# Kernel tuning notes

Measured on AMD Instinct MI355X. Metric: run time of the kernel, lower is better.

Reference implementation:

```python
import jax, jax.numpy as jnp
import numpy as np

NUM_HEADS = 16
HEAD_DIM = 64


def setup_inputs() -> dict:
    key = jax.random.key(0)
    ks = jax.random.split(key, 6)
    B, S, E = 4, 1024, 1024
    return {
        "x": jax.random.normal(ks[0], (B, S, E), dtype=jnp.float32),
        "W_qkv": jax.random.normal(ks[1], (E, 3 * E), dtype=jnp.float32) * 0.02,
        "b_qkv": jax.random.normal(ks[2], (3 * E,), dtype=jnp.float32) * 0.02,
        "pe": jax.random.normal(ks[3], (S, S, HEAD_DIM), dtype=jnp.float32) * 0.02,
        "W_out": jax.random.normal(ks[4], (E, E), dtype=jnp.float32) * 0.02,
        "b_out": jax.random.normal(ks[5], (E,), dtype=jnp.float32) * 0.02,
    }


def reference(x, W_qkv, b_qkv, pe, W_out, b_out):
    B, S, E = x.shape
    H, D = NUM_HEADS, HEAD_DIM
    scale = D ** -0.5
    # qkv projection: (B,S,3E) -> (3,B,H,S,D)
    qkv = (x @ W_qkv + b_qkv).reshape(B, S, 3, H, D).transpose(2, 0, 3, 1, 4)
    q, k, v = qkv[0], qkv[1], qkv[2]
    # raw scaled scores (NO softmax in original module)
    scores = jnp.einsum('bhxd,bhyd->bhxy', q, k) * scale
    # relative position bias: pe is (S,S,D) == (x,y,c); original permutes to (c,x,y)
    # then einsum('cxy,bnxc->bnxy', pe, q) -> equivalent to 'xyc,bhxc->bhxy'
    pe_q = jnp.einsum('xyc,bhxc->bhxy', pe, q) * scale
    attn = (scores + pe_q) @ v                      # (B,H,S,D)
    out = attn.transpose(0, 2, 1, 3).reshape(B, S, E)
    return out @ W_out + b_out
```

## Files before the change

### kernel.cpp

```cpp
#include <hip/hip_runtime.h>
#include <cstdint>
#include <cstddef>


typedef unsigned short u16;
typedef __bf16 bf16x8 __attribute__((ext_vector_type(8)));
typedef float  f32x4  __attribute__((ext_vector_type(4)));
typedef unsigned short u16x8 __attribute__((ext_vector_type(8)));

#define MFMA16(a, b, c) __builtin_amdgcn_mfma_f32_16x16x32_bf16((a), (b), (c), 0, 0, 0)

__device__ __forceinline__ u16 f2bf(float f) {
    __bf16 h = (__bf16)f;
    return __builtin_bit_cast(u16, h);
}
__device__ __forceinline__ float bf2f(u16 u) {
    unsigned int x = ((unsigned int)u) << 16;
    return __builtin_bit_cast(float, x);
}
__device__ __forceinline__ u16x8 pack8(float4 a, float4 b) {
    u16x8 v;
    v[0] = f2bf(a.x); v[1] = f2bf(a.y); v[2] = f2bf(a.z); v[3] = f2bf(a.w);
    v[4] = f2bf(b.x); v[5] = f2bf(b.y); v[6] = f2bf(b.z); v[7] = f2bf(b.w);
    return v;
}

__global__ __launch_bounds__(256) void kconv_T(const float* __restrict__ in,
                                               u16* __restrict__ out, int R, int C) {
    __shared__ float tile[64][68];
    const int t  = threadIdx.x;
    const int r0 = blockIdx.y * 64, c0 = blockIdx.x * 64;
    const int rr = t >> 4, c4 = t & 15;
    for (int p = 0; p < 4; ++p) {
        int r = rr + p * 16;
        float4 v = *(const float4*)&in[(size_t)(r0 + r) * C + c0 + c4 * 4];
        *(float4*)&tile[r][c4 * 4] = v;
    }
    __syncthreads();
    for (int p = 0; p < 4; ++p) {
        int n = rr + p * 16;
        ushort4 o;
        o.x = f2bf(tile[c4 * 4 + 0][n]);
        o.y = f2bf(tile[c4 * 4 + 1][n]);
        o.z = f2bf(tile[c4 * 4 + 2][n]);
        o.w = f2bf(tile[c4 * 4 + 3][n]);
        *(ushort4*)&out[(size_t)(c0 + n) * R + r0 + c4 * 4] = o;
    }
}

__global__ __launch_bounds__(256, 3) void kgemm_qkv(const float* __restrict__ X,
                                                    const u16* __restrict__ WT,
                                                    const float* __restrict__ bias,
                                                    u16* __restrict__ qb,
                                                    u16* __restrict__ kb,
                                                    u16* __restrict__ vb) {
    __shared__ u16 a_s[128 * 72];
    __shared__ u16 b_s[128 * 72];
    const int t = threadIdx.x;
    const int m0 = blockIdx.y * 128, n0 = blockIdx.x * 128;
    const int lane = t & 63, w = t >> 6, lm = lane & 15, lq = lane >> 4;
    const int mb = (w >> 1) * 64, nb = (w & 1) * 64;
    const int srow = t >> 3, scc = t & 7;

    f32x4 acc[4][4] = {};
    for (int k0 = 0; k0 < 1024; k0 += 64) {
        __syncthreads();
        for (int p = 0; p < 4; ++p) {
            int r = srow + p * 32;
            const float* src = &X[(size_t)(m0 + r) * 1024 + k0 + scc * 8];
            float4 f0 = *(const float4*)&src[0];
            float4 f1 = *(const float4*)&src[4];
            *(u16x8*)&a_s[r * 72 + scc * 8] = pack8(f0, f1);
        }
        for (int p = 0; p < 4; ++p) {
            int r = srow + p * 32;
            *(u16x8*)&b_s[r * 72 + scc * 8] =
                *(const u16x8*)&WT[(size_t)(n0 + r) * 1024 + k0 + scc * 8];
        }
        __syncthreads();
#pragma unroll
        for (int ks = 0; ks < 2; ++ks) {
            bf16x8 af[4], bfr[4];
#pragma unroll
            for (int mt = 0; mt < 4; ++mt)
                af[mt] = *(const bf16x8*)&a_s[(mb + mt * 16 + lm) * 72 + ks * 32 + lq * 8];
#pragma unroll
            for (int nt = 0; nt < 4; ++nt)
                bfr[nt] = *(const bf16x8*)&b_s[(nb + nt * 16 + lm) * 72 + ks * 32 + lq * 8];
#pragma unroll
            for (int mt = 0; mt < 4; ++mt)
#pragma unroll
                for (int nt = 0; nt < 4; ++nt)
                    acc[mt][nt] = MFMA16(af[mt], bfr[nt], acc[mt][nt]);
        }
    }
    for (int nt = 0; nt < 4; ++nt) {
        int col = n0 + nb + nt * 16 + lm;
        float bv = bias[col];
        int which = col >> 10;
        int h = (col >> 6) & 15, d = col & 63;
        u16* dst = (which == 0) ? qb : ((which == 1) ? kb : vb);
        for (int mt = 0; mt < 4; ++mt) {
            for (int i = 0; i < 4; ++i) {
                int row = m0 + mb + mt * 16 + lq * 4 + i;
                int b = row >> 10, s = row & 1023;
                dst[((size_t)((b * 16 + h) * 1024 + s)) * 64 + d] =
                    f2bf(acc[mt][nt][i] + bv);
            }
        }
    }
}

__global__ __launch_bounds__(256) void ktrans_v(const u16* __restrict__ v,
                                                u16* __restrict__ vt) {
    __shared__ u16 tv[64 * 72];
    const int bid = blockIdx.x;
    const int bh = bid >> 4, st = bid & 15;
    const int s0 = st * 64;
    const int t = threadIdx.x;
    const int rr = t >> 3, cc = t & 7;
    for (int p = 0; p < 2; ++p) {
        int s = rr + p * 32;
        *(u16x8*)&tv[s * 72 + cc * 8] =
            *(const u16x8*)&v[(size_t)(bh * 1024 + s0 + s) * 64 + cc * 8];
    }
    __syncthreads();
    for (int p = 0; p < 2; ++p) {
        int d = rr + p * 32;
        u16x8 o;
#pragma unroll
        for (int j = 0; j < 8; ++j) o[j] = tv[(cc * 8 + j) * 72 + d];
        *(u16x8*)&vt[(size_t)(bh * 64 + d) * 1024 + s0 + cc * 8] = o;
    }
}

__global__ __launch_bounds__(256, 2) void kpq(const u16* __restrict__ qb,
                                              const float* __restrict__ pe,
                                              u16* __restrict__ Pq) {
    __shared__ u16 q_s[64 * 72];
    __shared__ u16 pe_s[64 * 72];
    __shared__ u16 o_s[64 * 72];
    const int x = blockIdx.x;
    const int t = threadIdx.x;
    const int lane = t & 63, w = t >> 6, lm = lane & 15, lq = lane >> 4;
    {
        int rr = t >> 3, cc = t & 7;
        for (int p = 0; p < 2; ++p) {
            int bh = rr + p * 32;
            *(u16x8*)&q_s[bh * 72 + cc * 8] =
                *(const u16x8*)&qb[(size_t)(bh * 1024 + x) * 64 + cc * 8];
        }
    }
    const int yl = t >> 2, cq = t & 3;
    for (int y0 = 0; y0 < 1024; y0 += 64) {
        __syncthreads();
        {
            const float* src = &pe[(size_t)x * 65536 + (size_t)(y0 + yl) * 64 + cq * 16];
            float4 f0 = *(const float4*)&src[0];
            float4 f1 = *(const float4*)&src[4];
            float4 f2 = *(const float4*)&src[8];
            float4 f3 = *(const float4*)&src[12];
            *(u16x8*)&pe_s[yl * 72 + cq * 16]     = pack8(f0, f1);
            *(u16x8*)&pe_s[yl * 72 + cq * 16 + 8] = pack8(f2, f3);
        }
        __syncthreads();
        f32x4 acc[4] = {};
#pragma unroll
        for (int ks = 0; ks < 2; ++ks) {
            bf16x8 a = *(const bf16x8*)&pe_s[(16 * w + lm) * 72 + ks * 32 + lq * 8];
#pragma unroll
            for (int nt = 0; nt < 4; ++nt) {
                bf16x8 b = *(const bf16x8*)&q_s[(nt * 16 + lm) * 72 + ks * 32 + lq * 8];
                acc[nt] = MFMA16(a, b, acc[nt]);
            }
        }
#pragma unroll
        for (int nt = 0; nt < 4; ++nt) {
            ushort4 o;
            o.x = f2bf(acc[nt][0]); o.y = f2bf(acc[nt][1]);
            o.z = f2bf(acc[nt][2]); o.w = f2bf(acc[nt][3]);
            *(ushort4*)&o_s[(nt * 16 + lm) * 72 + 16 * w + lq * 4] = o;
        }
        __syncthreads();
        {
            int bh = t >> 2, yc = t & 3;
            u16x8 r0 = *(const u16x8*)&o_s[bh * 72 + yc * 16];
            u16x8 r1 = *(const u16x8*)&o_s[bh * 72 + yc * 16 + 8];
            size_t base = ((size_t)bh * 1024 + x) * 1024 + y0 + yc * 16;
            *(u16x8*)&Pq[base]     = r0;
            *(u16x8*)&Pq[base + 8] = r1;
        }
    }
}

__global__ __launch_bounds__(256, 2) void kattn(const u16* __restrict__ qb,
                                                const u16* __restrict__ kb,
                                                const u16* __restrict__ vt,
                                                const u16* __restrict__ Pq,
                                                u16* __restrict__ attnb) {
    __shared__ u16 q_s[128 * 72];
    __shared__ u16 k_s[64 * 72];
    __shared__ u16 v_s[64 * 72];
    __shared__ u16 s_s[128 * 72];
    const int bid = blockIdx.x;
    const int bh = bid >> 3, xt = bid & 7;
    const int x0 = xt * 128;
    const int t = threadIdx.x;
    const int lane = t & 63, w = t >> 6, lm = lane & 15, lq = lane >> 4;
    const int rr = t >> 3, cc = t & 7;

    for (int p = 0; p < 4; ++p) {
        int r = rr + p * 32;
        *(u16x8*)&q_s[r * 72 + cc * 8] =
            *(const u16x8*)&qb[(size_t)(bh * 1024 + x0 + r) * 64 + cc * 8];
    }
    f32x4 oacc[2][4] = {};
    for (int y0 = 0; y0 < 1024; y0 += 64) {
        __syncthreads();
        for (int p = 0; p < 2; ++p) {
            int r = rr + p * 32;
            *(u16x8*)&k_s[r * 72 + cc * 8] =
                *(const u16x8*)&kb[(size_t)(bh * 1024 + y0 + r) * 64 + cc * 8];
            *(u16x8*)&v_s[r * 72 + cc * 8] =
                *(const u16x8*)&vt[(size_t)(bh * 64 + r) * 1024 + y0 + cc * 8];
        }
        for (int p = 0; p < 4; ++p) {
            int r = rr + p * 32;
            *(u16x8*)&s_s[r * 72 + cc * 8] =
                *(const u16x8*)&Pq[((size_t)(bh * 1024 + x0 + r)) * 1024 + y0 + cc * 8];
        }
        __syncthreads();
        f32x4 sacc[4][2] = {};
#pragma unroll
        for (int ks = 0; ks < 2; ++ks) {
            bf16x8 bq[2];
#pragma unroll
            for (int nt = 0; nt < 2; ++nt)
                bq[nt] = *(const bf16x8*)&q_s[(32 * w + nt * 16 + lm) * 72 + ks * 32 + lq * 8];
#pragma unroll
            for (int mt = 0; mt < 4; ++mt) {
                bf16x8 ak = *(const bf16x8*)&k_s[(mt * 16 + lm) * 72 + ks * 32 + lq * 8];
#pragma unroll
                for (int nt = 0; nt < 2; ++nt)
                    sacc[mt][nt] = MFMA16(ak, bq[nt], sacc[mt][nt]);
            }
        }
#pragma unroll
        for (int nt = 0; nt < 2; ++nt) {
            int xl = 32 * w + nt * 16 + lm;
#pragma unroll
            for (int mt = 0; mt < 4; ++mt) {
                int yl = mt * 16 + lq * 4;
                ushort4 pq = *(const ushort4*)&s_s[xl * 72 + yl];
                ushort4 o;
                o.x = f2bf((sacc[mt][nt][0] + bf2f(pq.x)) * 0.125f);
                o.y = f2bf((sacc[mt][nt][1] + bf2f(pq.y)) * 0.125f);
                o.z = f2bf((sacc[mt][nt][2] + bf2f(pq.z)) * 0.125f);
                o.w = f2bf((sacc[mt][nt][3] + bf2f(pq.w)) * 0.125f);
                *(ushort4*)&s_s[xl * 72 + yl] = o;
            }
        }
#pragma unroll
        for (int ks = 0; ks < 2; ++ks) {
            bf16x8 as[2];
#pragma unroll
            for (int mt = 0; mt < 2; ++mt)
                as[mt] = *(const bf16x8*)&s_s[(32 * w + mt * 16 + lm) * 72 + ks * 32 + lq * 8];
#pragma unroll
            for (int nt = 0; nt < 4; ++nt) {
                bf16x8 bv = *(const bf16x8*)&v_s[(nt * 16 + lm) * 72 + ks * 32 + lq * 8];
#pragma unroll
                for (int mt = 0; mt < 2; ++mt)
                    oacc[mt][nt] = MFMA16(as[mt], bv, oacc[mt][nt]);
            }
        }
    }
    const int b = bh >> 4, h = bh & 15;
    for (int mt = 0; mt < 2; ++mt) {
        for (int nt = 0; nt < 4; ++nt) {
            int d = nt * 16 + lm;
            for (int i = 0; i < 4; ++i) {
                int s = x0 + 32 * w + mt * 16 + lq * 4 + i;
                attnb[((size_t)(b * 1024 + s)) * 1024 + h * 64 + d] = f2bf(oacc[mt][nt][i]);
            }
        }
    }
}

__global__ __launch_bounds__(256, 3) void kgemm_out(const u16* __restrict__ A,
                                                    const u16* __restrict__ WT,
                                                    const float* __restrict__ bias,
                                                    float* __restrict__ out) {
    __shared__ u16 a_s[128 * 72];
    __shared__ u16 b_s[128 * 72];
    const int t = threadIdx.x;
    const int m0 = blockIdx.y * 128, n0 = blockIdx.x * 128;
    const int lane = t & 63, w = t >> 6, lm = lane & 15, lq = lane >> 4;
    const int mb = (w >> 1) * 64, nb = (w & 1) * 64;
    const int srow = t >> 3, scc = t & 7;

    f32x4 acc[4][4] = {};
    for (int k0 = 0; k0 < 1024; k0 += 64) {
        __syncthreads();
        for (int p = 0; p < 4; ++p) {
            int r = srow + p * 32;
            *(u16x8*)&a_s[r * 72 + scc * 8] =
                *(const u16x8*)&A[(size_t)(m0 + r) * 1024 + k0 + scc * 8];
        }
        for (int p = 0; p < 4; ++p) {
            int r = srow + p * 32;
            *(u16x8*)&b_s[r * 72 + scc * 8] =
                *(const u16x8*)&WT[(size_t)(n0 + r) * 1024 + k0 + scc * 8];
        }
        __syncthreads();
#pragma unroll
        for (int ks = 0; ks < 2; ++ks) {
            bf16x8 af[4], bfr[4];
#pragma unroll
            for (int mt = 0; mt < 4; ++mt)
                af[mt] = *(const bf16x8*)&a_s[(mb + mt * 16 + lm) * 72 + ks * 32 + lq * 8];
#pragma unroll
            for (int nt = 0; nt < 4; ++nt)
                bfr[nt] = *(const bf16x8*)&b_s[(nb + nt * 16 + lm) * 72 + ks * 32 + lq * 8];
#pragma unroll
            for (int mt = 0; mt < 4; ++mt)
#pragma unroll
                for (int nt = 0; nt < 4; ++nt)
                    acc[mt][nt] = MFMA16(af[mt], bfr[nt], acc[mt][nt]);
        }
    }
    for (int nt = 0; nt < 4; ++nt) {
        int col = n0 + nb + nt * 16 + lm;
        float bv = bias[col];
        for (int mt = 0; mt < 4; ++mt) {
            for (int i = 0; i < 4; ++i) {
                int row = m0 + mb + mt * 16 + lq * 4 + i;
                out[(size_t)row * 1024 + col] = acc[mt][nt][i] + bv;
            }
        }
    }
}

extern "C" void kernel_launch(void* const* d_in, const int* in_sizes, int n_in,
                              void* d_out, int out_size, void* d_ws, size_t ws_size,
                              hipStream_t stream) {
    (void)in_sizes; (void)n_in; (void)out_size; (void)ws_size;
    const float* x    = (const float*)d_in[0];
    const float* Wqkv = (const float*)d_in[1];
    const float* bqkv = (const float*)d_in[2];
    const float* pe   = (const float*)d_in[3];
    const float* Wout = (const float*)d_in[4];
    const float* bout = (const float*)d_in[5];
    float* out = (float*)d_out;

    char* ws = (char*)d_ws;
    u16* wqkvT = (u16*)ws;  ws += (size_t)3072 * 1024 * 2;
    u16* woutT = (u16*)ws;  ws += (size_t)1024 * 1024 * 2;
    u16* qb    = (u16*)ws;  ws += (size_t)64 * 1024 * 64 * 2;
    u16* kb    = (u16*)ws;  ws += (size_t)64 * 1024 * 64 * 2;
    u16* vb    = (u16*)ws;  ws += (size_t)64 * 1024 * 64 * 2;
    u16* vtb   = (u16*)ws;  ws += (size_t)64 * 64 * 1024 * 2;
    u16* attnb = (u16*)ws;  ws += (size_t)4 * 1024 * 1024 * 2;
    u16* pq    = (u16*)ws;  ws += (size_t)64 * 1024 * 1024 * 2;

    kconv_T<<<dim3(48, 16), 256, 0, stream>>>(Wqkv, wqkvT, 1024, 3072);
    kconv_T<<<dim3(16, 16), 256, 0, stream>>>(Wout, woutT, 1024, 1024);
    kgemm_qkv<<<dim3(24, 32), 256, 0, stream>>>(x, wqkvT, bqkv, qb, kb, vb);
    ktrans_v<<<1024, 256, 0, stream>>>(vb, vtb);
    kpq<<<1024, 256, 0, stream>>>(qb, pe, pq);
    kattn<<<512, 256, 0, stream>>>(qb, kb, vtb, pq, attnb);
    kgemm_out<<<dim3(8, 32), 256, 0, stream>>>(attnb, woutT, bout, out);
}
```

Measured before the change: 601.0 us.

## Use direct global-to-LDS loads, pre-convert x, double-buffer pe, register-load Pq

```diff
diff --git a/kernel.cpp b/kernel.cpp
--- a/kernel.cpp
+++ b/kernel.cpp
@@ -9,6 +9,11 @@
 typedef unsigned short u16x8 __attribute__((ext_vector_type(8)));
 
 #define MFMA16(a, b, c) __builtin_amdgcn_mfma_f32_16x16x32_bf16((a), (b), (c), 0, 0, 0)
+
+#define GLOAD16(g, l)                                                        \
+    __builtin_amdgcn_global_load_lds(                                        \
+        (const __attribute__((address_space(1))) unsigned int*)(g),          \
+        (__attribute__((address_space(3))) unsigned int*)(l), 16, 0, 0)
 
 __device__ __forceinline__ u16 f2bf(float f) {
     __bf16 h = (__bf16)f;
@@ -23,6 +28,14 @@
     v[0] = f2bf(a.x); v[1] = f2bf(a.y); v[2] = f2bf(a.z); v[3] = f2bf(a.w);
     v[4] = f2bf(b.x); v[5] = f2bf(b.y); v[6] = f2bf(b.z); v[7] = f2bf(b.w);
     return v;
+}
+
+__global__ __launch_bounds__(256) void kxconv(const float* __restrict__ in,
+                                              u16* __restrict__ out) {
+    int i = (blockIdx.x * 256 + threadIdx.x) * 8;
+    float4 f0 = *(const float4*)&in[i];
+    float4 f1 = *(const float4*)&in[i + 4];
+    *(u16x8*)&out[i] = pack8(f0, f1);
 }
 
 __global__ __launch_bounds__(256) void kconv_T(const float* __restrict__ in,
@@ -48,34 +61,27 @@
     }
 }
 
-__global__ __launch_bounds__(256, 3) void kgemm_qkv(const float* __restrict__ X,
+__global__ __launch_bounds__(256, 2) void kgemm_qkv(const u16* __restrict__ A,
                                                     const u16* __restrict__ WT,
                                                     const float* __restrict__ bias,
                                                     u16* __restrict__ qb,
                                                     u16* __restrict__ kb,
                                                     u16* __restrict__ vb) {
-    __shared__ u16 a_s[128 * 72];
-    __shared__ u16 b_s[128 * 72];
+    __shared__ u16 a_s[128 * 64];
+    __shared__ u16 b_s[128 * 64];
     const int t = threadIdx.x;
     const int m0 = blockIdx.y * 128, n0 = blockIdx.x * 128;
     const int lane = t & 63, w = t >> 6, lm = lane & 15, lq = lane >> 4;
     const int mb = (w >> 1) * 64, nb = (w & 1) * 64;
-    const int srow = t >> 3, scc = t & 7;
+    const int sr = t >> 3, sc = (t & 7) * 8;
 
     f32x4 acc[4][4] = {};
     for (int k0 = 0; k0 < 1024; k0 += 64) {
         __syncthreads();
+#pragma unroll
         for (int p = 0; p < 4; ++p) {
-            int r = srow + p * 32;
-            const float* src = &X[(size_t)(m0 + r) * 1024 + k0 + scc * 8];
-            float4 f0 = *(const float4*)&src[0];
-            float4 f1 = *(const float4*)&src[4];
-            *(u16x8*)&a_s[r * 72 + scc * 8] = pack8(f0, f1);
-        }
-        for (int p = 0; p < 4; ++p) {
-            int r = srow + p * 32;
-            *(u16x8*)&b_s[r * 72 + scc * 8] =
-                *(const u16x8*)&WT[(size_t)(n0 + r) * 1024 + k0 + scc * 8];
+            GLOAD16(&A [(size_t)(m0 + p * 32 + sr) * 1024 + k0 + sc], &a_s[p * 2048 + t * 8]);
+            GLOAD16(&WT[(size_t)(n0 + p * 32 + sr) * 1024 + k0 + sc], &b_s[p * 2048 + t * 8]);
         }
         __syncthreads();
 #pragma unroll
@@ -83,10 +89,10 @@
             bf16x8 af[4], bfr[4];
 #pragma unroll
             for (int mt = 0; mt < 4; ++mt)
-                af[mt] = *(const bf16x8*)&a_s[(mb + mt * 16 + lm) * 72 + ks * 32 + lq * 8];
+                af[mt] = *(const bf16x8*)&a_s[(mb + mt * 16 + lm) * 64 + ks * 32 + lq * 8];
 #pragma unroll
             for (int nt = 0; nt < 4; ++nt)
-                bfr[nt] = *(const bf16x8*)&b_s[(nb + nt * 16 + lm) * 72 + ks * 32 + lq * 8];
+                bfr[nt] = *(const bf16x8*)&b_s[(nb + nt * 16 + lm) * 64 + ks * 32 + lq * 8];
 #pragma unroll
             for (int mt = 0; mt < 4; ++mt)
 #pragma unroll
@@ -115,8 +121,7 @@
                                                 u16* __restrict__ vt) {
     __shared__ u16 tv[64 * 72];
     const int bid = blockIdx.x;
-    const int bh = bid >> 4, st = bid & 15;
-    const int s0 = st * 64;
+    const int bh = bid >> 4, s0 = (bid & 15) * 64;
     const int t = threadIdx.x;
     const int rr = t >> 3, cc = t & 7;
     for (int p = 0; p < 2; ++p) {
@@ -137,40 +142,42 @@
 __global__ __launch_bounds__(256, 2) void kpq(const u16* __restrict__ qb,
                                               const float* __restrict__ pe,
                                               u16* __restrict__ Pq) {
-    __shared__ u16 q_s[64 * 72];
-    __shared__ u16 pe_s[64 * 72];
-    __shared__ u16 o_s[64 * 72];
+    __shared__ u16 q_s[64 * 64];
+    __shared__ u16 pe_s[2][64 * 80];
+    __shared__ u16 o_s[2][64 * 72];
     const int x = blockIdx.x;
     const int t = threadIdx.x;
     const int lane = t & 63, w = t >> 6, lm = lane & 15, lq = lane >> 4;
+#pragma unroll
+    for (int p = 0; p < 2; ++p)
+        GLOAD16(&qb[(size_t)((p * 32 + (t >> 3)) * 1024 + x) * 64 + (t & 7) * 8],
+                &q_s[p * 2048 + t * 8]);
+    const int yl = t >> 2, cq = (t & 3) * 16;
+    const float* pex = pe + (size_t)x * 65536;
+    float4 r0, r1, r2, r3;
     {
-        int rr = t >> 3, cc = t & 7;
-        for (int p = 0; p < 2; ++p) {
-            int bh = rr + p * 32;
-            *(u16x8*)&q_s[bh * 72 + cc * 8] =
-                *(const u16x8*)&qb[(size_t)(bh * 1024 + x) * 64 + cc * 8];
-        }
-    }
-    const int yl = t >> 2, cq = t & 3;
-    for (int y0 = 0; y0 < 1024; y0 += 64) {
-        __syncthreads();
-        {
-            const float* src = &pe[(size_t)x * 65536 + (size_t)(y0 + yl) * 64 + cq * 16];
-            float4 f0 = *(const float4*)&src[0];
-            float4 f1 = *(const float4*)&src[4];
-            float4 f2 = *(const float4*)&src[8];
-            float4 f3 = *(const float4*)&src[12];
-            *(u16x8*)&pe_s[yl * 72 + cq * 16]     = pack8(f0, f1);
-            *(u16x8*)&pe_s[yl * 72 + cq * 16 + 8] = pack8(f2, f3);
-        }
-        __syncthreads();
+        const float* src = &pex[(size_t)yl * 64 + cq];
+        r0 = *(const float4*)&src[0];  r1 = *(const float4*)&src[4];
+        r2 = *(const float4*)&src[8];  r3 = *(const float4*)&src[12];
+    }
+    int cur = 0;
+    const int obh = t >> 2, oyc = t & 3;
+    for (int it = 0; it < 16; ++it) {
+        *(u16x8*)&pe_s[cur][yl * 80 + cq]     = pack8(r0, r1);
+        *(u16x8*)&pe_s[cur][yl * 80 + cq + 8] = pack8(r2, r3);
+        __syncthreads();
+        if (it < 15) {
+            const float* src = &pex[(size_t)((it + 1) * 64 + yl) * 64 + cq];
+            r0 = *(const float4*)&src[0];  r1 = *(const float4*)&src[4];
+            r2 = *(const float4*)&src[8];  r3 = *(const float4*)&src[12];
+        }
         f32x4 acc[4] = {};
 #pragma unroll
         for (int ks = 0; ks < 2; ++ks) {
-            bf16x8 a = *(const bf16x8*)&pe_s[(16 * w + lm) * 72 + ks * 32 + lq * 8];
+            bf16x8 a = *(const bf16x8*)&pe_s[cur][(16 * w + lm) * 80 + ks * 32 + lq * 8];
 #pragma unroll
             for (int nt = 0; nt < 4; ++nt) {
-                bf16x8 b = *(const bf16x8*)&q_s[(nt * 16 + lm) * 72 + ks * 32 + lq * 8];
+                bf16x8 b = *(const bf16x8*)&q_s[(nt * 16 + lm) * 64 + ks * 32 + lq * 8];
                 acc[nt] = MFMA16(a, b, acc[nt]);
             }
         }
@@ -179,17 +186,17 @@
             ushort4 o;
             o.x = f2bf(acc[nt][0]); o.y = f2bf(acc[nt][1]);
             o.z = f2bf(acc[nt][2]); o.w = f2bf(acc[nt][3]);
-            *(ushort4*)&o_s[(nt * 16 + lm) * 72 + 16 * w + lq * 4] = o;
+            *(ushort4*)&o_s[cur][(nt * 16 + lm) * 72 + 16 * w + lq * 4] = o;
         }
         __syncthreads();
         {
-            int bh = t >> 2, yc = t & 3;
-            u16x8 r0 = *(const u16x8*)&o_s[bh * 72 + yc * 16];
-            u16x8 r1 = *(const u16x8*)&o_s[bh * 72 + yc * 16 + 8];
-            size_t base = ((size_t)bh * 1024 + x) * 1024 + y0 + yc * 16;
-            *(u16x8*)&Pq[base]     = r0;
-            *(u16x8*)&Pq[base + 8] = r1;
-        }
+            u16x8 a0 = *(const u16x8*)&o_s[cur][obh * 72 + oyc * 16];
+            u16x8 a1 = *(const u16x8*)&o_s[cur][obh * 72 + oyc * 16 + 8];
+            size_t base = ((size_t)obh * 1024 + x) * 1024 + it * 64 + oyc * 16;
+            *(u16x8*)&Pq[base]     = a0;
+            *(u16x8*)&Pq[base + 8] = a1;
+        }
+        cur ^= 1;
     }
 }
 
@@ -198,36 +205,37 @@
                                                 const u16* __restrict__ vt,
                                                 const u16* __restrict__ Pq,
                                                 u16* __restrict__ attnb) {
-    __shared__ u16 q_s[128 * 72];
-    __shared__ u16 k_s[64 * 72];
-    __shared__ u16 v_s[64 * 72];
-    __shared__ u16 s_s[128 * 72];
+    __shared__ u16 q_s[128 * 64];
+    __shared__ u16 k_s[64 * 64];
+    __shared__ u16 v_s[64 * 64];
+    __shared__ u16 s_s[128 * 80];
     const int bid = blockIdx.x;
-    const int bh = bid >> 3, xt = bid & 7;
-    const int x0 = xt * 128;
+    const int bh = bid >> 3, x0 = (bid & 7) * 128;
     const int t = threadIdx.x;
     const int lane = t & 63, w = t >> 6, lm = lane & 15, lq = lane >> 4;
-    const int rr = t >> 3, cc = t & 7;
-
-    for (int p = 0; p < 4; ++p) {
-        int r = rr + p * 32;
-        *(u16x8*)&q_s[r * 72 + cc * 8] =
-            *(const u16x8*)&qb[(size_t)(bh * 1024 + x0 + r) * 64 + cc * 8];
-    }
+    const int sr = t >> 3, sc = (t & 7) * 8;
+
+#pragma unroll
+    for (int p = 0; p < 4; ++p)
+        GLOAD16(&qb[(size_t)(bh * 1024 + x0 + p * 32 + sr) * 64 + sc],
+                &q_s[p * 2048 + t * 8]);
+
+    const u16* PqRow = Pq + ((size_t)(bh * 1024) + x0 + 32 * w + lm) * 1024 + lq * 4;
     f32x4 oacc[2][4] = {};
     for (int y0 = 0; y0 < 1024; y0 += 64) {
-        __syncthreads();
+        ushort4 pqr[4][2];
+#pragma unroll
+        for (int nt = 0; nt < 2; ++nt)
+#pragma unroll
+            for (int mt = 0; mt < 4; ++mt)
+                pqr[mt][nt] = *(const ushort4*)&PqRow[(size_t)(nt * 16) * 1024 + y0 + mt * 16];
+        __syncthreads();
+#pragma unroll
         for (int p = 0; p < 2; ++p) {
-            int r = rr + p * 32;
-            *(u16x8*)&k_s[r * 72 + cc * 8] =
-                *(const u16x8*)&kb[(size_t)(bh * 1024 + y0 + r) * 64 + cc * 8];
-            *(u16x8*)&v_s[r * 72 + cc * 8] =
-                *(const u16x8*)&vt[(size_t)(bh * 64 + r) * 1024 + y0 + cc * 8];
-        }
-        for (int p = 0; p < 4; ++p) {
-            int r = rr + p * 32;
-            *(u16x8*)&s_s[r * 72 + cc * 8] =
-                *(const u16x8*)&Pq[((size_t)(bh * 1024 + x0 + r)) * 1024 + y0 + cc * 8];
+            GLOAD16(&kb[(size_t)(bh * 1024 + y0 + p * 32 + sr) * 64 + sc],
+                    &k_s[p * 2048 + t * 8]);
+            GLOAD16(&vt[(size_t)(bh * 64 + p * 32 + sr) * 1024 + y0 + sc],
+                    &v_s[p * 2048 + t * 8]);
         }
         __syncthreads();
         f32x4 sacc[4][2] = {};
@@ -236,10 +244,10 @@
             bf16x8 bq[2];
 #pragma unroll
             for (int nt = 0; nt < 2; ++nt)
-                bq[nt] = *(const bf16x8*)&q_s[(32 * w + nt * 16 + lm) * 72 + ks * 32 + lq * 8];
+                bq[nt] = *(const bf16x8*)&q_s[(32 * w + nt * 16 + lm) * 64 + ks * 32 + lq * 8];
 #pragma unroll
             for (int mt = 0; mt < 4; ++mt) {
-                bf16x8 ak = *(const bf16x8*)&k_s[(mt * 16 + lm) * 72 + ks * 32 + lq * 8];
+                bf16x8 ak = *(const bf16x8*)&k_s[(mt * 16 + lm) * 64 + ks * 32 + lq * 8];
 #pragma unroll
                 for (int nt = 0; nt < 2; ++nt)
                     sacc[mt][nt] = MFMA16(ak, bq[nt], sacc[mt][nt]);
@@ -250,14 +258,13 @@
             int xl = 32 * w + nt * 16 + lm;
 #pragma unroll
             for (int mt = 0; mt < 4; ++mt) {
-                int yl = mt * 16 + lq * 4;
-                ushort4 pq = *(const ushort4*)&s_s[xl * 72 + yl];
+                ushort4 pq = pqr[mt][nt];
                 ushort4 o;
                 o.x = f2bf((sacc[mt][nt][0] + bf2f(pq.x)) * 0.125f);
                 o.y = f2bf((sacc[mt][nt][1] + bf2f(pq.y)) * 0.125f);
                 o.z = f2bf((sacc[mt][nt][2] + bf2f(pq.z)) * 0.125f);
                 o.w = f2bf((sacc[mt][nt][3] + bf2f(pq.w)) * 0.125f);
-                *(ushort4*)&s_s[xl * 72 + yl] = o;
+                *(ushort4*)&s_s[xl * 80 + mt * 16 + lq * 4] = o;
             }
         }
 #pragma unroll
@@ -265,10 +272,10 @@
             bf16x8 as[2];
 #pragma unroll
             for (int mt = 0; mt < 2; ++mt)
-                as[mt] = *(const bf16x8*)&s_s[(32 * w + mt * 16 + lm) * 72 + ks * 32 + lq * 8];
+                as[mt] = *(const bf16x8*)&s_s[(32 * w + mt * 16 + lm) * 80 + ks * 32 + lq * 8];
 #pragma unroll
             for (int nt = 0; nt < 4; ++nt) {
-                bf16x8 bv = *(const bf16x8*)&v_s[(nt * 16 + lm) * 72 + ks * 32 + lq * 8];
+                bf16x8 bv = *(const bf16x8*)&v_s[(nt * 16 + lm) * 64 + ks * 32 + lq * 8];
 #pragma unroll
                 for (int mt = 0; mt < 2; ++mt)
                     oacc[mt][nt] = MFMA16(as[mt], bv, oacc[mt][nt]);
@@ -287,30 +294,25 @@
     }
 }
 
-__global__ __launch_bounds__(256, 3) void kgemm_out(const u16* __restrict__ A,
+__global__ __launch_bounds__(256, 2) void kgemm_out(const u16* __restrict__ A,
                                                     const u16* __restrict__ WT,
                                                     const float* __restrict__ bias,
                                                     float* __restrict__ out) {
-    __shared__ u16 a_s[128 * 72];
-    __shared__ u16 b_s[128 * 72];
+    __shared__ u16 a_s[128 * 64];
+    __shared__ u16 b_s[128 * 64];
     const int t = threadIdx.x;
     const int m0 = blockIdx.y * 128, n0 = blockIdx.x * 128;
     const int lane = t & 63, w = t >> 6, lm = lane & 15, lq = lane >> 4;
     const int mb = (w >> 1) * 64, nb = (w & 1) * 64;
-    const int srow = t >> 3, scc = t & 7;
+    const int sr = t >> 3, sc = (t & 7) * 8;
 
     f32x4 acc[4][4] = {};
     for (int k0 = 0; k0 < 1024; k0 += 64) {
         __syncthreads();
+#pragma unroll
         for (int p = 0; p < 4; ++p) {
-            int r = srow + p * 32;
-            *(u16x8*)&a_s[r * 72 + scc * 8] =
-                *(const u16x8*)&A[(size_t)(m0 + r) * 1024 + k0 + scc * 8];
-        }
-        for (int p = 0; p < 4; ++p) {
-            int r = srow + p * 32;
-            *(u16x8*)&b_s[r * 72 + scc * 8] =
-                *(const u16x8*)&WT[(size_t)(n0 + r) * 1024 + k0 + scc * 8];
+            GLOAD16(&A [(size_t)(m0 + p * 32 + sr) * 1024 + k0 + sc], &a_s[p * 2048 + t * 8]);
+            GLOAD16(&WT[(size_t)(n0 + p * 32 + sr) * 1024 + k0 + sc], &b_s[p * 2048 + t * 8]);
         }
         __syncthreads();
 #pragma unroll
@@ -318,10 +320,10 @@
             bf16x8 af[4], bfr[4];
 #pragma unroll
             for (int mt = 0; mt < 4; ++mt)
-                af[mt] = *(const bf16x8*)&a_s[(mb + mt * 16 + lm) * 72 + ks * 32 + lq * 8];
+                af[mt] = *(const bf16x8*)&a_s[(mb + mt * 16 + lm) * 64 + ks * 32 + lq * 8];
 #pragma unroll
             for (int nt = 0; nt < 4; ++nt)
-                bfr[nt] = *(const bf16x8*)&b_s[(nb + nt * 16 + lm) * 72 + ks * 32 + lq * 8];
+                bfr[nt] = *(const bf16x8*)&b_s[(nb + nt * 16 + lm) * 64 + ks * 32 + lq * 8];
 #pragma unroll
             for (int mt = 0; mt < 4; ++mt)
 #pragma unroll
@@ -354,6 +356,7 @@
     float* out = (float*)d_out;
 
     char* ws = (char*)d_ws;
+    u16* xb    = (u16*)ws;  ws += (size_t)4096 * 1024 * 2;
     u16* wqkvT = (u16*)ws;  ws += (size_t)3072 * 1024 * 2;
     u16* woutT = (u16*)ws;  ws += (size_t)1024 * 1024 * 2;
     u16* qb    = (u16*)ws;  ws += (size_t)64 * 1024 * 64 * 2;
@@ -363,9 +366,10 @@
     u16* attnb = (u16*)ws;  ws += (size_t)4 * 1024 * 1024 * 2;
     u16* pq    = (u16*)ws;  ws += (size_t)64 * 1024 * 1024 * 2;
 
+    kxconv<<<2048, 256, 0, stream>>>(x, xb);
     kconv_T<<<dim3(48, 16), 256, 0, stream>>>(Wqkv, wqkvT, 1024, 3072);
     kconv_T<<<dim3(16, 16), 256, 0, stream>>>(Wout, woutT, 1024, 1024);
-    kgemm_qkv<<<dim3(24, 32), 256, 0, stream>>>(x, wqkvT, bqkv, qb, kb, vb);
+    kgemm_qkv<<<dim3(24, 32), 256, 0, stream>>>(xb, wqkvT, bqkv, qb, kb, vb);
     ktrans_v<<<1024, 256, 0, stream>>>(vb, vtb);
     kpq<<<1024, 256, 0, stream>>>(qb, pe, pq);
     kattn<<<512, 256, 0, stream>>>(qb, kb, vtb, pq, attnb);
```

Measured after the change: 543.3 us. 1.11x faster.
